# Kernel tuning notes

Measured on AMD Instinct MI355X. Metric: run time of the kernel, lower is better.

The kernel has to match this reference:

```python
import jax, jax.numpy as jnp
import numpy as np

NUM_CLASS = 20
ALPHA = 1.0
BETA = 1.0
IGNORE = 255


def _fdiff(f, ax):
    """np.gradient/torch.gradient with unit spacing along axis ax (edge_order=1)."""
    n = f.shape[ax]
    sl = lambda a, b: jax.lax.slice_in_dim(f, a, b, axis=ax)
    interior = (sl(2, n) - sl(0, n - 2)) * 0.5
    first = sl(1, 2) - sl(0, 1)
    last = sl(n - 1, n) - sl(n - 2, n - 1)
    return jnp.concatenate([first, interior, last], axis=ax)


def _lga(targets):
    # one-hot over all classes at once: [C, B, D, H, W]
    cls = jnp.arange(NUM_CLASS, dtype=targets.dtype)[:, None, None, None, None]
    oh = (targets[None] == cls).astype(jnp.float32)
    res = jnp.zeros(targets.shape, jnp.float32)
    for ax in (2, 3, 4):  # spatial dims of [C,B,D,H,W]
        res = res + jnp.sum(jnp.abs(_fdiff(oh, ax)), axis=0)
    return res  # [B, D, H, W]


def setup_inputs() -> dict:
    key = jax.random.key(0)
    k1, k2, k3, k4 = jax.random.split(key, 4)
    B, D, H, W = 1, 256, 256, 32
    predictions = jax.random.normal(k1, (B, NUM_CLASS, D, H, W), dtype=jnp.float32)
    targets = jax.random.randint(k2, (B, D, H, W), 0, NUM_CLASS)
    ignore = jax.random.uniform(k3, (B, D, H, W)) < 0.02
    targets = jnp.where(ignore, IGNORE, targets).astype(jnp.int32)
    class_weights = jax.random.uniform(k4, (NUM_CLASS,), dtype=jnp.float32) + 0.1
    return {"predictions": predictions, "targets": targets, "class_weights": class_weights}


def reference(predictions, targets, class_weights):
    targets = targets.astype(jnp.int32)
    valid = targets != IGNORE
    t = jnp.where(valid, targets, 0)
    # weighted CE, reduction='none': -w[t] * log_softmax(pred)[t], 0 at ignore
    logp = jax.nn.log_softmax(predictions, axis=1)
    logp_t = jnp.take_along_axis(logp, t[:, None], axis=1)[:, 0]  # [B,D,H,W]
    w = class_weights[t]
    loss = jnp.where(valid, -w * logp_t, 0.0)
    lga_weights = ALPHA + BETA * _lga(targets)
    num = jnp.sum(loss * lga_weights)
    den = jnp.sum(jnp.where(valid, w, 0.0))
    return num / den
```

## Files before the change

kernel.cpp:

```cpp
#include <hip/hip_runtime.h>

#define NUM_CLASS 20
#define IGNORE_V 255
#define WW 32
#define HH 256
#define DDEPTH 256
#define NVOX (DDEPTH * HH * WW)

__device__ __forceinline__ float fpair(int a, int b) {
    if (a == b) return 0.0f;
    return (a == IGNORE_V || b == IGNORE_V) ? 1.0f : 2.0f;
}

__global__ void pal_init(float* acc) {
    acc[0] = 0.0f;
    acc[1] = 0.0f;
}

__global__ __launch_bounds__(256) void pal_main(
    const float* __restrict__ pred,
    const int*   __restrict__ tgt,
    const float* __restrict__ cw,
    float*       __restrict__ acc)
{
    const int gid = blockIdx.x * blockDim.x + threadIdx.x;
    const int v0  = gid * 4;

    int4 t4 = *reinterpret_cast<const int4*>(tgt + v0);
    int t[4] = {t4.x, t4.y, t4.z, t4.w};

    float m[4], s[4], pt[4];
    {
        float4 x = *reinterpret_cast<const float4*>(pred + v0);
        float xx[4] = {x.x, x.y, x.z, x.w};
        #pragma unroll
        for (int j = 0; j < 4; j++) {
            m[j] = xx[j];
            s[j] = 1.0f;
            pt[j] = (t[j] == 0) ? xx[j] : 0.0f;
        }
    }
    #pragma unroll
    for (int c = 1; c < NUM_CLASS; c++) {
        float4 x = *reinterpret_cast<const float4*>(pred + (size_t)c * NVOX + v0);
        float xx[4] = {x.x, x.y, x.z, x.w};
        #pragma unroll
        for (int j = 0; j < 4; j++) {
            float nm = fmaxf(m[j], xx[j]);
            s[j] = s[j] * __expf(m[j] - nm) + __expf(xx[j] - nm);
            m[j] = nm;
            if (t[j] == c) pt[j] = xx[j];
        }
    }

    float num = 0.0f, den = 0.0f;
    #pragma unroll
    for (int j = 0; j < 4; j++) {
        const int v = v0 + j;
        const int w = v & (WW - 1);
        const int h = (v >> 5) & (HH - 1);
        const int d = v >> 13;
        float lga = 0.0f;
        {
            int im = v - ((w == 0) ? 0 : 1);
            int ip = v + ((w == WW - 1) ? 0 : 1);
            float sc = (w == 0 || w == WW - 1) ? 1.0f : 0.5f;
            lga += sc * fpair(tgt[im], tgt[ip]);
        }
        {
            int im = v - ((h == 0) ? 0 : WW);
            int ip = v + ((h == HH - 1) ? 0 : WW);
            float sc = (h == 0 || h == HH - 1) ? 1.0f : 0.5f;
            lga += sc * fpair(tgt[im], tgt[ip]);
        }
        {
            int im = v - ((d == 0) ? 0 : WW * HH);
            int ip = v + ((d == DDEPTH - 1) ? 0 : WW * HH);
            float sc = (d == 0 || d == DDEPTH - 1) ? 1.0f : 0.5f;
            lga += sc * fpair(tgt[im], tgt[ip]);
        }
        const int tj = t[j];
        if (tj != IGNORE_V) {
            float wt  = cw[tj];
            float lse = m[j] + __logf(s[j]);
            num += wt * (lse - pt[j]) * (1.0f + lga);
            den += wt;
        }
    }

    #pragma unroll
    for (int off = 32; off > 0; off >>= 1) {
        num += __shfl_down(num, off);
        den += __shfl_down(den, off);
    }
    __shared__ float sn[4], sd[4];
    const int lane = threadIdx.x & 63;
    const int wid  = threadIdx.x >> 6;
    if (lane == 0) { sn[wid] = num; sd[wid] = den; }
    __syncthreads();
    if (threadIdx.x == 0) {
        float n = sn[0] + sn[1] + sn[2] + sn[3];
        float d2 = sd[0] + sd[1] + sd[2] + sd[3];
        atomicAdd(&acc[0], n);
        atomicAdd(&acc[1], d2);
    }
}

__global__ void pal_final(const float* acc, float* out) {
    out[0] = acc[0] / acc[1];
}

extern "C" void kernel_launch(void* const* d_in, const int* in_sizes, int n_in,
                              void* d_out, int out_size, void* d_ws, size_t ws_size,
                              hipStream_t stream) {
    const float* pred = (const float*)d_in[0];
    const int*   tgt  = (const int*)d_in[1];
    const float* cw   = (const float*)d_in[2];
    float* out = (float*)d_out;
    float* acc = (float*)d_ws;

    pal_init<<<1, 1, 0, stream>>>(acc);
    const int threads = 256;
    const int blocks  = (NVOX / 4) / threads;
    pal_main<<<blocks, threads, 0, stream>>>(pred, tgt, cw, acc);
    pal_final<<<1, 1, 0, stream>>>(acc, out);
}
```

Before: 258.3 us.

## Process eight voxels per thread, drop online max, fuse final division

Each thread now handles eight voxels and issues batched float4 loads of five classes at a time. The online max rescaling in softmax is removed in favour of a plain exp-sum. The neighbour-target lookups become vectorised int4 loads with in-register W-neighbours, and class weights are staged in shared memory. The separate final kernel is replaced by a last-block ticket, which saves one launch. Dropping the max subtraction risks overflow for large logits.

```diff
diff --git a/kernel.cpp b/kernel.cpp
--- a/kernel.cpp
+++ b/kernel.cpp
@@ -8,82 +8,109 @@
 #define NVOX (DDEPTH * HH * WW)
 
 __device__ __forceinline__ float fpair(int a, int b) {
-    if (a == b) return 0.0f;
-    return (a == IGNORE_V || b == IGNORE_V) ? 1.0f : 2.0f;
+    return (a == b) ? 0.0f : ((a == IGNORE_V || b == IGNORE_V) ? 1.0f : 2.0f);
 }
 
 __global__ void pal_init(float* acc) {
     acc[0] = 0.0f;
     acc[1] = 0.0f;
+    ((unsigned*)acc)[2] = 0u;
 }
 
 __global__ __launch_bounds__(256) void pal_main(
     const float* __restrict__ pred,
     const int*   __restrict__ tgt,
     const float* __restrict__ cw,
-    float*       __restrict__ acc)
+    float*       __restrict__ acc,
+    float*       __restrict__ out)
 {
+    __shared__ float lcw[NUM_CLASS];
+    if (threadIdx.x < NUM_CLASS) lcw[threadIdx.x] = cw[threadIdx.x];
+    __syncthreads();
+
     const int gid = blockIdx.x * blockDim.x + threadIdx.x;
-    const int v0  = gid * 4;
+    const int v0  = gid * 8;
+    const int w0  = v0 & (WW - 1);
+    const int h   = (v0 >> 5) & (HH - 1);
+    const int d   = v0 >> 13;
 
-    int4 t4 = *reinterpret_cast<const int4*>(tgt + v0);
-    int t[4] = {t4.x, t4.y, t4.z, t4.w};
+    int4 ta = *reinterpret_cast<const int4*>(tgt + v0);
+    int4 tb = *reinterpret_cast<const int4*>(tgt + v0 + 4);
+    int t[8] = {ta.x, ta.y, ta.z, ta.w, tb.x, tb.y, tb.z, tb.w};
 
-    float m[4], s[4], pt[4];
-    {
-        float4 x = *reinterpret_cast<const float4*>(pred + v0);
-        float xx[4] = {x.x, x.y, x.z, x.w};
+    float s[8]  = {0,0,0,0,0,0,0,0};
+    float pt[8] = {0,0,0,0,0,0,0,0};
+    const float* pb = pred + v0;
+    #pragma unroll
+    for (int cc = 0; cc < NUM_CLASS; cc += 5) {
+        float4 xa[5], xb[5];
         #pragma unroll
-        for (int j = 0; j < 4; j++) {
-            m[j] = xx[j];
-            s[j] = 1.0f;
-            pt[j] = (t[j] == 0) ? xx[j] : 0.0f;
+        for (int k = 0; k < 5; k++) {
+            const float* p = pb + (size_t)(cc + k) * NVOX;
+            xa[k] = *reinterpret_cast<const float4*>(p);
+            xb[k] = *reinterpret_cast<const float4*>(p + 4);
+        }
+        #pragma unroll
+        for (int k = 0; k < 5; k++) {
+            const int c = cc + k;
+            float xx[8] = {xa[k].x, xa[k].y, xa[k].z, xa[k].w,
+                           xb[k].x, xb[k].y, xb[k].z, xb[k].w};
+            #pragma unroll
+            for (int j = 0; j < 8; j++) {
+                s[j] += __expf(xx[j]);
+                if (t[j] == c) pt[j] = xx[j];
+            }
         }
     }
-    #pragma unroll
-    for (int c = 1; c < NUM_CLASS; c++) {
-        float4 x = *reinterpret_cast<const float4*>(pred + (size_t)c * NVOX + v0);
-        float xx[4] = {x.x, x.y, x.z, x.w};
+
+    float lga[8];
+    {
+        int tm1 = tgt[v0 - ((w0 != 0) ? 1 : 0)];
+        int tp8 = tgt[v0 + 7 + ((w0 != WW - 8) ? 1 : 0)];
         #pragma unroll
-        for (int j = 0; j < 4; j++) {
-            float nm = fmaxf(m[j], xx[j]);
-            s[j] = s[j] * __expf(m[j] - nm) + __expf(xx[j] - nm);
-            m[j] = nm;
-            if (t[j] == c) pt[j] = xx[j];
+        for (int j = 0; j < 8; j++) {
+            const int wj = w0 + j;
+            int tL = (j > 0) ? t[j-1] : ((w0 == 0)      ? t[0] : tm1);
+            int tR = (j < 7) ? t[j+1] : ((w0 == WW - 8) ? t[7] : tp8);
+            float sc = (wj == 0 || wj == WW - 1) ? 1.0f : 0.5f;
+            lga[j] = sc * fpair(tL, tR);
         }
+    }
+    {
+        const int up = v0 - ((h != 0)      ? WW : 0);
+        const int dn = v0 + ((h != HH - 1) ? WW : 0);
+        int4 ua = *reinterpret_cast<const int4*>(tgt + up);
+        int4 ub = *reinterpret_cast<const int4*>(tgt + up + 4);
+        int4 da = *reinterpret_cast<const int4*>(tgt + dn);
+        int4 db = *reinterpret_cast<const int4*>(tgt + dn + 4);
+        int tu[8] = {ua.x, ua.y, ua.z, ua.w, ub.x, ub.y, ub.z, ub.w};
+        int td[8] = {da.x, da.y, da.z, da.w, db.x, db.y, db.z, db.w};
+        const float sc = (h == 0 || h == HH - 1) ? 1.0f : 0.5f;
+        #pragma unroll
+        for (int j = 0; j < 8; j++) lga[j] += sc * fpair(tu[j], td[j]);
+    }
+    {
+        const int bk = v0 - ((d != 0)          ? WW * HH : 0);
+        const int fr = v0 + ((d != DDEPTH - 1) ? WW * HH : 0);
+        int4 ba = *reinterpret_cast<const int4*>(tgt + bk);
+        int4 bb = *reinterpret_cast<const int4*>(tgt + bk + 4);
+        int4 fa = *reinterpret_cast<const int4*>(tgt + fr);
+        int4 fb = *reinterpret_cast<const int4*>(tgt + fr + 4);
+        int tB[8] = {ba.x, ba.y, ba.z, ba.w, bb.x, bb.y, bb.z, bb.w};
+        int tF[8] = {fa.x, fa.y, fa.z, fa.w, fb.x, fb.y, fb.z, fb.w};
+        const float sc = (d == 0 || d == DDEPTH - 1) ? 1.0f : 0.5f;
+        #pragma unroll
+        for (int j = 0; j < 8; j++) lga[j] += sc * fpair(tB[j], tF[j]);
     }
 
     float num = 0.0f, den = 0.0f;
     #pragma unroll
-    for (int j = 0; j < 4; j++) {
-        const int v = v0 + j;
-        const int w = v & (WW - 1);
-        const int h = (v >> 5) & (HH - 1);
-        const int d = v >> 13;
-        float lga = 0.0f;
-        {
-            int im = v - ((w == 0) ? 0 : 1);
-            int ip = v + ((w == WW - 1) ? 0 : 1);
-            float sc = (w == 0 || w == WW - 1) ? 1.0f : 0.5f;
-            lga += sc * fpair(tgt[im], tgt[ip]);
-        }
-        {
-            int im = v - ((h == 0) ? 0 : WW);
-            int ip = v + ((h == HH - 1) ? 0 : WW);
-            float sc = (h == 0 || h == HH - 1) ? 1.0f : 0.5f;
-            lga += sc * fpair(tgt[im], tgt[ip]);
-        }
-        {
-            int im = v - ((d == 0) ? 0 : WW * HH);
-            int ip = v + ((d == DDEPTH - 1) ? 0 : WW * HH);
-            float sc = (d == 0 || d == DDEPTH - 1) ? 1.0f : 0.5f;
-            lga += sc * fpair(tgt[im], tgt[ip]);
-        }
+    for (int j = 0; j < 8; j++) {
         const int tj = t[j];
         if (tj != IGNORE_V) {
-            float wt  = cw[tj];
-            float lse = m[j] + __logf(s[j]);
-            num += wt * (lse - pt[j]) * (1.0f + lga);
+            const float wt  = lcw[tj];
+            const float lse = __logf(s[j]);
+            num += wt * (lse - pt[j]) * (1.0f + lga[j]);
             den += wt;
         }
     }
@@ -99,15 +126,18 @@
     if (lane == 0) { sn[wid] = num; sd[wid] = den; }
     __syncthreads();
     if (threadIdx.x == 0) {
-        float n = sn[0] + sn[1] + sn[2] + sn[3];
+        float n  = sn[0] + sn[1] + sn[2] + sn[3];
         float d2 = sd[0] + sd[1] + sd[2] + sd[3];
         atomicAdd(&acc[0], n);
         atomicAdd(&acc[1], d2);
+        __threadfence();
+        unsigned ticket = atomicAdd((unsigned*)&acc[2], 1u);
+        if (ticket == gridDim.x - 1) {
+            float fn = atomicAdd(&acc[0], 0.0f);
+            float fd = atomicAdd(&acc[1], 0.0f);
+            out[0] = fn / fd;
+        }
     }
-}
-
-__global__ void pal_final(const float* acc, float* out) {
-    out[0] = acc[0] / acc[1];
 }
 
 extern "C" void kernel_launch(void* const* d_in, const int* in_sizes, int n_in,
@@ -121,7 +151,6 @@
 
     pal_init<<<1, 1, 0, stream>>>(acc);
     const int threads = 256;
-    const int blocks  = (NVOX / 4) / threads;
-    pal_main<<<blocks, threads, 0, stream>>>(pred, tgt, cw, acc);
-    pal_final<<<1, 1, 0, stream>>>(acc, out);
+    const int blocks  = (NVOX / 8) / threads;
+    pal_main<<<blocks, threads, 0, stream>>>(pred, tgt, cw, acc, out);
 }
```

Result: slower. 283.0 us (+9.6%).
